# Performance work log

Measured on AMD Instinct MI355X. Metric: run time of the kernel, lower is better.

## Reference

```python
import jax, jax.numpy as jnp
import numpy as np
import math

B, SQ, SK = 8, 1024, 1024
DQ = DK = DV = 1024
H = 16
EPS = 1e-5


def _layer_norm(x, g, b):
    mu = jnp.mean(x, axis=-1, keepdims=True)
    var = jnp.mean(jnp.square(x - mu), axis=-1, keepdims=True)
    return (x - mu) * jax.lax.rsqrt(var + EPS) * g + b


def setup_inputs() -> dict:
    key = jax.random.key(0)
    ks = jax.random.split(key, 8)
    s_q = 1.0 / math.sqrt(DQ)
    s_v = 1.0 / math.sqrt(DV)
    return {
        "Q": jax.random.normal(ks[0], (B, SQ, DQ), dtype=jnp.float32),
        "K": jax.random.normal(ks[1], (B, SK, DK), dtype=jnp.float32),
        "Wq": jax.random.normal(ks[2], (DQ, DV), dtype=jnp.float32) * s_q,
        "bq": jnp.zeros((DV,), dtype=jnp.float32),
        "Wk": jax.random.normal(ks[3], (DK, DV), dtype=jnp.float32) * s_q,
        "bk": jnp.zeros((DV,), dtype=jnp.float32),
        "Wv": jax.random.normal(ks[4], (DK, DV), dtype=jnp.float32) * s_q,
        "bv": jnp.zeros((DV,), dtype=jnp.float32),
        "Wo": jax.random.normal(ks[5], (DV, DV), dtype=jnp.float32) * s_v,
        "bo": jnp.zeros((DV,), dtype=jnp.float32),
        "g0": jnp.ones((DV,), dtype=jnp.float32),
        "b0": jnp.zeros((DV,), dtype=jnp.float32),
        "g1": jnp.ones((DV,), dtype=jnp.float32),
        "b1": jnp.zeros((DV,), dtype=jnp.float32),
    }


def reference(Q, K, Wq, bq, Wk, bk, Wv, bv, Wo, bo, g0, b0, g1, b1):
    dh = DV // H
    q = Q @ Wq + bq                      # [B,SQ,DV]
    k = K @ Wk + bk                      # [B,SK,DV]
    v = K @ Wv + bv                      # [B,SK,DV]
    # split/cat over heads == reshape to [B,S,H,dh]
    qh = q.reshape(B, SQ, H, dh)
    kh = k.reshape(B, SK, H, dh)
    vh = v.reshape(B, SK, H, dh)
    # NOTE: original scales by sqrt(dim_V), not sqrt(head_dim)
    scores = jnp.einsum("bqhd,bkhd->bhqk", qh, kh) / math.sqrt(DV)
    A = jax.nn.softmax(scores, axis=-1)  # [B,H,SQ,SK]
    attn = jnp.einsum("bhqk,bkhd->bqhd", A, vh)
    out = q + attn.reshape(B, SQ, DV)    # residual with projected Q
    out = _layer_norm(out, g0, b0)
    out = out + jax.nn.relu(out @ Wo + bo)
    out = _layer_norm(out, g1, b1)
    return out
```

## Files before the change

### kernel.cpp

```cpp
#include <hip/hip_runtime.h>
#include <hip/hip_bf16.h>
#include <stdint.h>

#define NB 8
#define NSQ 1024
#define NSK 1024
#define ND 1024
#define NH 16
#define NDH 64
#define NM (NB * NSQ)
#define LOG2E 1.4426950408889634f

typedef __bf16 bf16;
typedef __bf16 bf16x8 __attribute__((ext_vector_type(8)));
typedef float f32x4 __attribute__((ext_vector_type(4)));
typedef float f32x16 __attribute__((ext_vector_type(16)));
typedef unsigned int uint32;

__device__ __forceinline__ void async_load16(const void* g, void* l) {
  __builtin_amdgcn_global_load_lds(
      (__attribute__((address_space(1))) void*)g,
      (__attribute__((address_space(3))) void*)l, 16, 0, 0);
}

__device__ __forceinline__ void permswap(uint32& x, uint32& y) {
#if __has_builtin(__builtin_amdgcn_permlane32_swap)
  auto r = __builtin_amdgcn_permlane32_swap(x, y, false, false);
  x = r[0]; y = r[1];
#else
  asm volatile("v_permlane32_swap_b32 %0, %1" : "+v"(x), "+v"(y));
#endif
}

__global__ __launch_bounds__(256) void cvt2_f32_bf16(const float* __restrict__ A,
                                                     const float* __restrict__ B,
                                                     bf16* __restrict__ Oa,
                                                     bf16* __restrict__ Ob) {
  const float* in = blockIdx.y ? B : A;
  bf16* out = blockIdx.y ? Ob : Oa;
  int i = blockIdx.x * 256 + threadIdx.x;
  float4 v = *(const float4*)(in + (size_t)i * 4);
  union { uint64_t u; bf16 h[4]; } o;
  o.h[0] = (bf16)v.x; o.h[1] = (bf16)v.y; o.h[2] = (bf16)v.z; o.h[3] = (bf16)v.w;
  *(uint64_t*)(out + (size_t)i * 4) = o.u;
}

__global__ __launch_bounds__(256) void transpose_cvt4(
    const float* __restrict__ W0, const float* __restrict__ W1,
    const float* __restrict__ W2, const float* __restrict__ W3,
    bf16* __restrict__ O0, bf16* __restrict__ O1,
    bf16* __restrict__ O2, bf16* __restrict__ O3) {
  const float* W; bf16* Wt;
  switch (blockIdx.z) {
    case 0: W = W0; Wt = O0; break;
    case 1: W = W1; Wt = O1; break;
    case 2: W = W2; Wt = O2; break;
    default: W = W3; Wt = O3; break;
  }
  __shared__ float t[64][65];
  const int bc = blockIdx.x * 64;
  const int br = blockIdx.y * 64;
  const int tid = threadIdx.x;
  for (int c = tid; c < 1024; c += 256) {
    int r = c >> 4, off = (c & 15) * 4;
    float4 v = *(const float4*)&W[(size_t)(br + r) * 1024 + bc + off];
    t[r][off] = v.x; t[r][off + 1] = v.y; t[r][off + 2] = v.z; t[r][off + 3] = v.w;
  }
  __syncthreads();
  for (int c = tid; c < 512; c += 256) {
    int cc = c >> 3, rr = (c & 7) * 8;
    union { uint4 u; bf16 h[8]; } o;
#pragma unroll
    for (int i = 0; i < 8; ++i) o.h[i] = (bf16)t[rr + i][cc];
    *(uint4*)&Wt[(size_t)(bc + cc) * 1024 + br + rr] = o.u;
  }
}

__global__ __launch_bounds__(256) void transpose_v(const bf16* __restrict__ vsrc,
                                                   bf16* __restrict__ vT) {
  const int st = blockIdx.x * 64;
  const int bh = blockIdx.y;
  const int b = bh >> 4, h = bh & 15;
  __shared__ __align__(16) bf16 t[64][72];
  const int tid = threadIdx.x;
  for (int c = tid; c < 512; c += 256) {
    int s = c >> 3, off = (c & 7) * 8;
    *(uint4*)&t[s][off] =
        *(const uint4*)&vsrc[(size_t)(b * NSK + st + s) * 2048 + 1024 + h * NDH + off];
  }
  __syncthreads();
  for (int c = tid; c < 512; c += 256) {
    int d = c >> 3, s0 = (c & 7) * 8;
    union { uint4 u; bf16 h[8]; } o;
#pragma unroll
    for (int i = 0; i < 8; ++i) o.h[i] = t[s0 + i][d];
    *(uint4*)&vT[((size_t)(bh * NDH + d)) * NSK + st + s0] = o.u;
  }
}

template <int BM, int MODE, int NXC>
__global__ __launch_bounds__(256, 2) void gemm3b(
    const bf16* __restrict__ A, const bf16* __restrict__ Bt,
    const float* __restrict__ bias, const float* __restrict__ bias2,
    bf16* __restrict__ Cb, const bf16* __restrict__ Resb, float scale, int N) {
  constexpr int NT = 32;
  constexpr int AR = BM / 64;
  constexpr int MR = BM / 32;
  __shared__ __align__(16) bf16 Asl[3][BM * 32];
  __shared__ __align__(16) bf16 Bsl[3][128 * 32];

  const int tid = threadIdx.x;
  const int flat = blockIdx.x;
  const int xi = (flat & 7) * 64 + (flat >> 3);
  const int bcol = (xi & (NXC - 1)) * 128;
  const int brow = (xi / NXC) * BM;

  const int w = tid >> 6, lane = tid & 63;
  const int wm = w >> 1, wn = w & 1;
  const int lr = lane & 15, l4 = lane >> 4;
  const int rgrp = l4 * 4;
  const int gph = (l4 ^ ((lr >> 1) & 3)) * 8;

  const int srow = tid >> 2;
  const int gsrc = (tid & 3) ^ ((tid >> 3) & 3);
  const bf16* Ag = A + (size_t)(brow + srow) * 1024 + gsrc * 8;
  const bf16* Bg = Bt + (size_t)(bcol + srow) * 1024 + gsrc * 8;
  const int ldo = srow * 32 + (tid & 3) * 8;

  auto stage = [&](int d, int kt) {
#pragma unroll
    for (int r = 0; r < AR; ++r)
      async_load16(Ag + (size_t)r * (64 * 1024) + kt * 32, &Asl[d][r * 2048 + ldo]);
#pragma unroll
    for (int r = 0; r < 2; ++r)
      async_load16(Bg + (size_t)r * (64 * 1024) + kt * 32, &Bsl[d][r * 2048 + ldo]);
  };
  auto wait_tile = [&]() {
    if constexpr (BM == 256) asm volatile("s_waitcnt vmcnt(6)" ::: "memory");
    else                     asm volatile("s_waitcnt vmcnt(4)" ::: "memory");
  };

  f32x4 acc[MR][4] = {};

  stage(0, 0);
  stage(1, 1);
  wait_tile();
  __builtin_amdgcn_s_barrier();

  int cur = 0, st2 = 2;
  for (int t = 0; t < NT; ++t) {
    bf16x8 af[MR], bfr[4];
#pragma unroll
    for (int i = 0; i < MR; ++i)
      af[i] = *(const bf16x8*)&Asl[cur][(wm * (BM / 2) + i * 16 + lr) * 32 + gph];
#pragma unroll
    for (int n = 0; n < 4; ++n)
      bfr[n] = *(const bf16x8*)&Bsl[cur][(wn * 64 + n * 16 + lr) * 32 + gph];
    if (t + 2 < NT) stage(st2, t + 2);
    asm volatile("s_waitcnt lgkmcnt(0)" ::: "memory");
    __builtin_amdgcn_sched_barrier(0);
    __builtin_amdgcn_s_setprio(1);
#pragma unroll
    for (int i = 0; i < MR; ++i)
#pragma unroll
      for (int n = 0; n < 4; ++n)
        acc[i][n] = __builtin_amdgcn_mfma_f32_16x16x32_bf16(af[i], bfr[n], acc[i][n], 0, 0, 0);
    __builtin_amdgcn_s_setprio(0);
    if (t + 2 < NT)      wait_tile();
    else if (t + 1 < NT) asm volatile("s_waitcnt vmcnt(0)" ::: "memory");
    __builtin_amdgcn_s_barrier();
    cur = (cur == 2) ? 0 : cur + 1;
    st2 = (st2 == 2) ? 0 : st2 + 1;
  }

#pragma unroll
  for (int m = 0; m < MR; ++m) {
#pragma unroll
    for (int n = 0; n < 4; ++n) {
      const int col = bcol + wn * 64 + n * 16 + lr;
      float bv, sc;
      if (MODE == 2) {
        const bool isV = (bcol >= 1024);
        bv = isV ? bias2[col - 1024] : bias[col];
        sc = isV ? 1.0f : LOG2E;
      } else {
        bv = bias[col];
        sc = scale;
      }
#pragma unroll
      for (int r = 0; r < 4; ++r) {
        const int row = brow + wm * (BM / 2) + m * 16 + rgrp + r;
        float v = acc[m][n][r] + bv;
        if (MODE == 1) {
          float res = (float)Resb[(size_t)row * N + col];
          Cb[(size_t)row * N + col] = (bf16)(res + (v > 0.f ? v : 0.f));
        } else {
          Cb[(size_t)row * N + col] = (bf16)(v * sc);
        }
      }
    }
  }
}

__global__ __launch_bounds__(512, 4) void attn_kernel(
    const bf16* __restrict__ qb, const bf16* __restrict__ kvb,
    const bf16* __restrict__ vT, bf16* __restrict__ attnout) {
  const int bh = blockIdx.y;
  const int b = bh >> 4, h = bh & 15;
  const int tid = threadIdx.x, w = tid >> 6, lane = tid & 63;
  const int l31 = lane & 31;
  const int l1 = lane >> 5;
  const int q0w = blockIdx.x * 256 + w * 32;

  __shared__ __align__(16) bf16 Kl[2][64 * 64];
  __shared__ __align__(16) bf16 Vl[2][64 * 64];

  const int srow = tid >> 3;
  const int sgran = tid & 7;
  const int gsw = sgran ^ (srow & 7);
  const int ldst = srow * 64 + sgran * 8;
  const int rg = l31 & 7;

  const bf16* kbase = kvb + (size_t)(b * NSK) * 2048 + h * NDH;
  const bf16* vbase = vT + (size_t)(bh * NDH) * NSK;

  bf16x8 qf[4];
#pragma unroll
  for (int kd = 0; kd < 4; ++kd)
    qf[kd] = *(const bf16x8*)&qb[(size_t)(b * NSQ + q0w + l31) * ND +
                                 h * NDH + kd * 16 + l1 * 8];

  f32x16 oacc0 = {}, oacc1 = {}, lacc = {};
  bf16x8 ones;
#pragma unroll
  for (int i = 0; i < 8; ++i) ones[i] = (bf16)1.0f;

  auto stage = [&](int bi, int kt) {
    async_load16(kbase + (size_t)(kt + srow) * 2048 + gsw * 8, &Kl[bi][ldst]);
    async_load16(vbase + (size_t)srow * NSK + kt + gsw * 8, &Vl[bi][ldst]);
  };

  stage(0, 0);

  for (int t = 0; t < 16; ++t) {
    const int bi = t & 1;
    asm volatile("s_waitcnt vmcnt(0)" ::: "memory");
    __syncthreads();
    if (t < 15) stage(bi ^ 1, (t + 1) * 64);

    uint32 W[2][4][2];
#pragma unroll
    for (int n = 0; n < 2; ++n) {
      f32x16 s = {};
      __builtin_amdgcn_s_setprio(1);
#pragma unroll
      for (int kd = 0; kd < 4; ++kd) {
        bf16x8 kf = *(const bf16x8*)&Kl[bi][(n * 32 + l31) * 64 + (((kd * 2 + l1) ^ rg) * 8)];
        s = __builtin_amdgcn_mfma_f32_32x32x16_bf16(kf, qf[kd], s, 0, 0, 0);
      }
      __builtin_amdgcn_s_setprio(0);
#pragma unroll
      for (int r2 = 0; r2 < 4; ++r2)
#pragma unroll
        for (int p = 0; p < 2; ++p) {
          float elo = __builtin_amdgcn_exp2f(s[r2 * 4 + 2 * p]);
          float ehi = __builtin_amdgcn_exp2f(s[r2 * 4 + 2 * p + 1]);
          uint32 wd;
          asm("v_cvt_pk_bf16_f32 %0, %1, %2" : "=v"(wd) : "v"(elo), "v"(ehi));
          W[n][r2][p] = wd;
        }
    }
    __builtin_amdgcn_s_setprio(1);
#pragma unroll
    for (int kc = 0; kc < 4; ++kc) {
      uint32 x0 = W[kc >> 1][(kc & 1) * 2][0], y0 = W[kc >> 1][(kc & 1) * 2 + 1][0];
      uint32 x1 = W[kc >> 1][(kc & 1) * 2][1], y1 = W[kc >> 1][(kc & 1) * 2 + 1][1];
      permswap(x0, y0);
      permswap(x1, y1);
      union { uint32 u[4]; bf16x8 v; } cvt;
      cvt.u[0] = x0; cvt.u[1] = x1; cvt.u[2] = y0; cvt.u[3] = y1;
      bf16x8 pa = cvt.v;
      bf16x8 vf0 = *(const bf16x8*)&Vl[bi][(l31) * 64 + (((kc * 2 + l1) ^ rg) * 8)];
      bf16x8 vf1 = *(const bf16x8*)&Vl[bi][(32 + l31) * 64 + (((kc * 2 + l1) ^ rg) * 8)];
      oacc0 = __builtin_amdgcn_mfma_f32_32x32x16_bf16(pa, vf0, oacc0, 0, 0, 0);
      oacc1 = __builtin_amdgcn_mfma_f32_32x32x16_bf16(pa, vf1, oacc1, 0, 0, 0);
      lacc = __builtin_amdgcn_mfma_f32_32x32x16_bf16(pa, ones, lacc, 0, 0, 0);
    }
    __builtin_amdgcn_s_setprio(0);
  }

  float inv[16];
#pragma unroll
  for (int r = 0; r < 16; ++r) inv[r] = 1.0f / lacc[r];
#pragma unroll
  for (int r = 0; r < 16; ++r) {
    const int row = q0w + (r & 3) + 8 * (r >> 2) + 4 * l1;
    attnout[(size_t)(b * NSQ + row) * ND + h * NDH + l31] = (bf16)(oacc0[r] * inv[r]);
    attnout[(size_t)(b * NSQ + row) * ND + h * NDH + 32 + l31] = (bf16)(oacc1[r] * inv[r]);
  }
}

template <bool RES, bool OUTF>
__global__ __launch_bounds__(256) void ln_kernel(
    const bf16* __restrict__ x, const bf16* __restrict__ rq, float rscale,
    const float* __restrict__ g, const float* __restrict__ be,
    bf16* __restrict__ yb, float* __restrict__ yf) {
  __shared__ float sm[4];
  const int row = blockIdx.x, tid = threadIdx.x;
  const size_t base = (size_t)row * ND + tid * 4;
  union { uint2 u; bf16 h[4]; } xv;
  xv.u = *(const uint2*)(x + base);
  float v0 = (float)xv.h[0], v1 = (float)xv.h[1], v2 = (float)xv.h[2], v3 = (float)xv.h[3];
  if (RES) {
    union { uint2 u; bf16 h[4]; } q;
    q.u = *(const uint2*)(rq + base);
    v0 += rscale * (float)q.h[0]; v1 += rscale * (float)q.h[1];
    v2 += rscale * (float)q.h[2]; v3 += rscale * (float)q.h[3];
  }
  float s = v0 + v1 + v2 + v3;
#pragma unroll
  for (int off = 32; off > 0; off >>= 1) s += __shfl_down(s, off, 64);
  if ((tid & 63) == 0) sm[tid >> 6] = s;
  __syncthreads();
  const float mean = (sm[0] + sm[1] + sm[2] + sm[3]) * (1.0f / ND);
  __syncthreads();
  const float d0 = v0 - mean, d1 = v1 - mean, d2 = v2 - mean, d3 = v3 - mean;
  float sq = d0 * d0 + d1 * d1 + d2 * d2 + d3 * d3;
#pragma unroll
  for (int off = 32; off > 0; off >>= 1) sq += __shfl_down(sq, off, 64);
  if ((tid & 63) == 0) sm[tid >> 6] = sq;
  __syncthreads();
  const float var = (sm[0] + sm[1] + sm[2] + sm[3]) * (1.0f / ND);
  const float rs = rsqrtf(var + 1e-5f);
  float4 gv = *(const float4*)(g + tid * 4);
  float4 bv = *(const float4*)(be + tid * 4);
  const float y0 = d0 * rs * gv.x + bv.x;
  const float y1 = d1 * rs * gv.y + bv.y;
  const float y2 = d2 * rs * gv.z + bv.z;
  const float y3 = d3 * rs * gv.w + bv.w;
  if (OUTF) {
    *(float4*)(yf + base) = make_float4(y0, y1, y2, y3);
  } else {
    union { uint2 u; bf16 h[4]; } o;
    o.h[0] = (bf16)y0; o.h[1] = (bf16)y1; o.h[2] = (bf16)y2; o.h[3] = (bf16)y3;
    *(uint2*)(yb + base) = o.u;
  }
}

extern "C" void kernel_launch(void* const* d_in, const int* in_sizes, int n_in,
                              void* d_out, int out_size, void* d_ws, size_t ws_size,
                              hipStream_t stream) {
  const float* Q  = (const float*)d_in[0];
  const float* K  = (const float*)d_in[1];
  const float* Wq = (const float*)d_in[2];
  const float* bq = (const float*)d_in[3];
  const float* Wk = (const float*)d_in[4];
  const float* bk = (const float*)d_in[5];
  const float* Wv = (const float*)d_in[6];
  const float* bv = (const float*)d_in[7];
  const float* Wo = (const float*)d_in[8];
  const float* bo = (const float*)d_in[9];
  const float* g0 = (const float*)d_in[10];
  const float* b0 = (const float*)d_in[11];
  const float* g1 = (const float*)d_in[12];
  const float* b1 = (const float*)d_in[13];
  float* out = (float*)d_out;

  char* ws = (char*)d_ws;
  const size_t MB = 1024 * 1024;
  bf16* Qb    = (bf16*)(ws + 0);
  bf16* Kb    = (bf16*)(ws + 16 * MB);
  bf16* Wqt   = (bf16*)(ws + 32 * MB);
  bf16* Wkvt  = (bf16*)(ws + 34 * MB);
  bf16* Wot   = (bf16*)(ws + 38 * MB);
  bf16* qb    = (bf16*)(ws + 40 * MB);
  bf16* kvb   = (bf16*)(ws + 56 * MB);
  bf16* vT    = (bf16*)(ws + 88 * MB);
  bf16* attnb = (bf16*)(ws + 104 * MB);
  bf16* h0b   = (bf16*)(ws + 56 * MB);
  bf16* out1b = (bf16*)(ws + 0);

  cvt2_f32_bf16<<<dim3(8192, 2), 256, 0, stream>>>(Q, K, Qb, Kb);
  transpose_cvt4<<<dim3(16, 16, 4), 256, 0, stream>>>(
      Wq, Wk, Wv, Wo, Wqt, Wkvt, Wkvt + 1024 * 1024, Wot);
  gemm3b<256, 2, 16><<<512, 256, 0, stream>>>(Kb, Wkvt, bk, bv, kvb, nullptr, 1.0f, 2048);
  gemm3b<128, 0, 8><<<512, 256, 0, stream>>>(Qb, Wqt, bq, nullptr, qb, nullptr, 0.03125f, 1024);
  transpose_v<<<dim3(16, 128), 256, 0, stream>>>(kvb, vT);
  attn_kernel<<<dim3(4, 128), 512, 0, stream>>>(qb, kvb, vT, attnb);
  ln_kernel<true, false><<<8192, 256, 0, stream>>>(attnb, qb, 32.0f, g0, b0, h0b, nullptr);
  gemm3b<128, 1, 8><<<512, 256, 0, stream>>>(h0b, Wot, bo, nullptr, out1b, h0b, 1.0f, 1024);
  ln_kernel<false, true><<<8192, 256, 0, stream>>>(out1b, nullptr, 0.f, g1, b1, nullptr, out);
}
```

Before: 180.1 us.

## Add 256x256 8-wave ping-pong GEMM for fused K/V projection

Replaces the K/V projection GEMM with a new 512-thread kernel that computes 256x256 tiles using a 64-wide K step and XOR-swizzled LDS. It interleaves LDS fragment reads, staged async global loads and four MFMA quadrants per iteration with barriers. The existing gemm3b also moves its LDS wait from before the MFMAs to the loop end, so fragment reads can overlap compute. The big tile needs 128KB of LDS per block, which limits occupancy, and the barrier schedule is intricate.

```diff
diff --git a/kernel.cpp b/kernel.cpp
--- a/kernel.cpp
+++ b/kernel.cpp
@@ -98,6 +98,157 @@
   }
 }
 
+__global__ __launch_bounds__(512, 2) void gemm8x(
+    const bf16* __restrict__ A, const bf16* __restrict__ Bt,
+    const float* __restrict__ bk_, const float* __restrict__ bv_,
+    bf16* __restrict__ Cb) {
+  constexpr int NT = 16;
+  __shared__ __align__(16) bf16 As[2][256 * 64];
+  __shared__ __align__(16) bf16 Bs[2][256 * 64];
+
+  const int flat = blockIdx.x;
+  const int xi = (flat & 7) * 32 + (flat >> 3);
+  const int bcol = (xi & 7) * 256;
+  const int brow = (xi >> 3) * 256;
+
+  const int tid = threadIdx.x;
+  const int w = tid >> 6, lane = tid & 63;
+  const int wm = w >> 2, wn = w & 3;
+  const int lr = lane & 15, l4 = lane >> 4;
+  const int rgrp = l4 * 4;
+  const int rx = lr & 7;
+
+  const int srow = tid >> 3;
+  const int sg = tid & 7;
+  const int gsw = sg ^ (srow & 7);
+  const bf16* Ag = A + (size_t)(brow + srow) * 1024 + gsw * 8;
+  const bf16* Bg = Bt + (size_t)(bcol + srow) * 1024 + gsw * 8;
+  const int ldso = srow * 64 + sg * 8;
+
+  auto stA = [&](int d, int h, int kt) {
+#pragma unroll
+    for (int r = 0; r < 2; ++r)
+      async_load16(Ag + (size_t)(h * 128 + r * 64) * 1024 + kt * 64,
+                   &As[d][(h * 128 + r * 64) * 64 + ldso]);
+  };
+  auto stB = [&](int d, int h, int kt) {
+#pragma unroll
+    for (int r = 0; r < 2; ++r)
+      async_load16(Bg + (size_t)(h * 128 + r * 64) * 1024 + kt * 64,
+                   &Bs[d][(h * 128 + r * 64) * 64 + ldso]);
+  };
+
+  f32x4 acc[8][4] = {};
+  bf16x8 af[4][2], bf0[2][2], bf1[2][2];
+
+  stA(0, 0, 0); stA(0, 1, 0); stB(0, 0, 0); stB(0, 1, 0);
+  stA(1, 0, 1);
+  asm volatile("s_waitcnt vmcnt(2)" ::: "memory");
+  __builtin_amdgcn_s_barrier();
+
+  for (int m = 0; m < NT; ++m) {
+    const int cur = m & 1, nxt = cur ^ 1;
+    const int arow = wm * 128;
+#pragma unroll
+    for (int i = 0; i < 4; ++i)
+#pragma unroll
+      for (int ks = 0; ks < 2; ++ks)
+        af[i][ks] = *(const bf16x8*)&As[cur][(arow + i * 16 + lr) * 64 +
+                                            (((ks * 4 + l4) ^ rx) * 8)];
+#pragma unroll
+    for (int nf = 0; nf < 2; ++nf)
+#pragma unroll
+      for (int ks = 0; ks < 2; ++ks)
+        bf0[nf][ks] = *(const bf16x8*)&Bs[cur][(wn * 64 + nf * 16 + lr) * 64 +
+                                              (((ks * 4 + l4) ^ rx) * 8)];
+    if (m + 1 < NT) stA(nxt, 1, m + 1);
+    __builtin_amdgcn_s_barrier();
+    asm volatile("s_waitcnt lgkmcnt(0)" ::: "memory");
+    __builtin_amdgcn_sched_barrier(0);
+    __builtin_amdgcn_s_setprio(1);
+#pragma unroll
+    for (int i = 0; i < 4; ++i)
+#pragma unroll
+      for (int nf = 0; nf < 2; ++nf)
+#pragma unroll
+        for (int ks = 0; ks < 2; ++ks)
+          acc[i][nf] = __builtin_amdgcn_mfma_f32_16x16x32_bf16(af[i][ks], bf0[nf][ks], acc[i][nf], 0, 0, 0);
+    __builtin_amdgcn_s_setprio(0);
+    __builtin_amdgcn_s_barrier();
+#pragma unroll
+    for (int nf = 0; nf < 2; ++nf)
+#pragma unroll
+      for (int ks = 0; ks < 2; ++ks)
+        bf1[nf][ks] = *(const bf16x8*)&Bs[cur][(wn * 64 + (2 + nf) * 16 + lr) * 64 +
+                                              (((ks * 4 + l4) ^ rx) * 8)];
+    if (m + 1 < NT) stB(nxt, 0, m + 1);
+    __builtin_amdgcn_s_barrier();
+    asm volatile("s_waitcnt lgkmcnt(0)" ::: "memory");
+    __builtin_amdgcn_sched_barrier(0);
+    __builtin_amdgcn_s_setprio(1);
+#pragma unroll
+    for (int i = 0; i < 4; ++i)
+#pragma unroll
+      for (int nf = 0; nf < 2; ++nf)
+#pragma unroll
+        for (int ks = 0; ks < 2; ++ks)
+          acc[i][2 + nf] = __builtin_amdgcn_mfma_f32_16x16x32_bf16(af[i][ks], bf1[nf][ks], acc[i][2 + nf], 0, 0, 0);
+    __builtin_amdgcn_s_setprio(0);
+    __builtin_amdgcn_s_barrier();
+#pragma unroll
+    for (int i = 0; i < 4; ++i)
+#pragma unroll
+      for (int ks = 0; ks < 2; ++ks)
+        af[i][ks] = *(const bf16x8*)&As[cur][(arow + 64 + i * 16 + lr) * 64 +
+                                            (((ks * 4 + l4) ^ rx) * 8)];
+    if (m + 1 < NT) stB(nxt, 1, m + 1);
+    __builtin_amdgcn_s_barrier();
+    asm volatile("s_waitcnt lgkmcnt(0)" ::: "memory");
+    __builtin_amdgcn_sched_barrier(0);
+    __builtin_amdgcn_s_setprio(1);
+#pragma unroll
+    for (int i = 0; i < 4; ++i)
+#pragma unroll
+      for (int nf = 0; nf < 2; ++nf)
+#pragma unroll
+        for (int ks = 0; ks < 2; ++ks)
+          acc[4 + i][nf] = __builtin_amdgcn_mfma_f32_16x16x32_bf16(af[i][ks], bf0[nf][ks], acc[4 + i][nf], 0, 0, 0);
+    __builtin_amdgcn_s_setprio(0);
+    __builtin_amdgcn_s_barrier();
+    if (m + 2 < NT) stA(cur, 0, m + 2);
+    __builtin_amdgcn_s_barrier();
+    __builtin_amdgcn_s_setprio(1);
+#pragma unroll
+    for (int i = 0; i < 4; ++i)
+#pragma unroll
+      for (int nf = 0; nf < 2; ++nf)
+#pragma unroll
+        for (int ks = 0; ks < 2; ++ks)
+          acc[4 + i][2 + nf] = __builtin_amdgcn_mfma_f32_16x16x32_bf16(af[i][ks], bf1[nf][ks], acc[4 + i][2 + nf], 0, 0, 0);
+    __builtin_amdgcn_s_setprio(0);
+    if (m + 2 < NT)      asm volatile("s_waitcnt vmcnt(2)" ::: "memory");
+    else if (m + 1 < NT) asm volatile("s_waitcnt vmcnt(0)" ::: "memory");
+    __builtin_amdgcn_s_barrier();
+  }
+
+  const bool isV = (bcol >= 1024);
+#pragma unroll
+  for (int q = 0; q < 2; ++q)
+#pragma unroll
+    for (int i = 0; i < 4; ++i)
+#pragma unroll
+      for (int n = 0; n < 4; ++n) {
+        const int col = bcol + wn * 64 + n * 16 + lr;
+        const float bvv = isV ? bv_[col - 1024] : bk_[col];
+        const float sc = isV ? 1.0f : LOG2E;
+#pragma unroll
+        for (int r = 0; r < 4; ++r) {
+          const int row = brow + wm * 128 + q * 64 + i * 16 + rgrp + r;
+          Cb[(size_t)row * 2048 + col] = (bf16)((acc[q * 4 + i][n][r] + bvv) * sc);
+        }
+      }
+}
+
 template <int BM, int MODE, int NXC>
 __global__ __launch_bounds__(256, 2) void gemm3b(
     const bf16* __restrict__ A, const bf16* __restrict__ Bt,
@@ -157,8 +308,6 @@
     for (int n = 0; n < 4; ++n)
       bfr[n] = *(const bf16x8*)&Bsl[cur][(wn * 64 + n * 16 + lr) * 32 + gph];
     if (t + 2 < NT) stage(st2, t + 2);
-    asm volatile("s_waitcnt lgkmcnt(0)" ::: "memory");
-    __builtin_amdgcn_sched_barrier(0);
     __builtin_amdgcn_s_setprio(1);
 #pragma unroll
     for (int i = 0; i < MR; ++i)
@@ -168,6 +317,7 @@
     __builtin_amdgcn_s_setprio(0);
     if (t + 2 < NT)      wait_tile();
     else if (t + 1 < NT) asm volatile("s_waitcnt vmcnt(0)" ::: "memory");
+    asm volatile("s_waitcnt lgkmcnt(0)" ::: "memory");
     __builtin_amdgcn_s_barrier();
     cur = (cur == 2) ? 0 : cur + 1;
     st2 = (st2 == 2) ? 0 : st2 + 1;
@@ -178,15 +328,7 @@
 #pragma unroll
     for (int n = 0; n < 4; ++n) {
       const int col = bcol + wn * 64 + n * 16 + lr;
-      float bv, sc;
-      if (MODE == 2) {
-        const bool isV = (bcol >= 1024);
-        bv = isV ? bias2[col - 1024] : bias[col];
-        sc = isV ? 1.0f : LOG2E;
-      } else {
-        bv = bias[col];
-        sc = scale;
-      }
+      const float bv = bias[col];
 #pragma unroll
       for (int r = 0; r < 4; ++r) {
         const int row = brow + wm * (BM / 2) + m * 16 + rgrp + r;
@@ -195,7 +337,7 @@
           float res = (float)Resb[(size_t)row * N + col];
           Cb[(size_t)row * N + col] = (bf16)(res + (v > 0.f ? v : 0.f));
         } else {
-          Cb[(size_t)row * N + col] = (bf16)(v * sc);
+          Cb[(size_t)row * N + col] = (bf16)(v * scale);
         }
       }
     }
@@ -383,7 +525,7 @@
   cvt2_f32_bf16<<<dim3(8192, 2), 256, 0, stream>>>(Q, K, Qb, Kb);
   transpose_cvt4<<<dim3(16, 16, 4), 256, 0, stream>>>(
       Wq, Wk, Wv, Wo, Wqt, Wkvt, Wkvt + 1024 * 1024, Wot);
-  gemm3b<256, 2, 16><<<512, 256, 0, stream>>>(Kb, Wkvt, bk, bv, kvb, nullptr, 1.0f, 2048);
+  gemm8x<<<256, 512, 0, stream>>>(Kb, Wkvt, bk, bv, kvb);
   gemm3b<128, 0, 8><<<512, 256, 0, stream>>>(Qb, Wqt, bq, nullptr, qb, nullptr, 0.03125f, 1024);
   transpose_v<<<dim3(16, 128), 256, 0, stream>>>(kvb, vT);
   attn_kernel<<<dim3(4, 128), 512, 0, stream>>>(qb, kvb, vT, attnb);
```

Measured after the change: 178.1 us. About the same (-1.1%).
